# Performance work log

Hardware: AMD Instinct MI355X
Metric: run time of the kernel (lower is better)

## Reference

```python
import jax, jax.numpy as jnp
import numpy as np

B, S, D, H = 2, 2048, 1024, 16
HD = D // H

def setup_inputs() -> dict:
    key = jax.random.key(0)
    k1, k2, k3, k4, k5 = jax.random.split(key, 5)
    X = jax.random.normal(k1, (B, S, D), dtype=jnp.float32)
    # nn.Linear(D, 3D): weight [3D, D], bias [3D]
    W_qkv = jax.random.normal(k2, (3 * D, D), dtype=jnp.float32) * (1.0 / np.sqrt(D))
    b_qkv = jax.random.normal(k3, (3 * D,), dtype=jnp.float32) * 0.02
    W_out = jax.random.normal(k4, (D, D), dtype=jnp.float32) * (1.0 / np.sqrt(D))
    b_out = jax.random.normal(k5, (D,), dtype=jnp.float32) * 0.02
    return {"X": X, "W_qkv": W_qkv, "b_qkv": b_qkv, "W_out": W_out, "b_out": b_out}

def reference(X, W_qkv, b_qkv, W_out, b_out):
    b, s, d = X.shape
    qkv = jnp.einsum('bsd,ed->bse', X, W_qkv) + b_qkv  # [B,S,3D]
    q, k, v = jnp.split(qkv, 3, axis=2)
    def heads(t):
        return t.reshape(b, s, H, HD).transpose(0, 2, 1, 3)  # [B,H,S,HD]
    q, k, v = heads(q), heads(k), heads(v)
    scores = jnp.einsum('bhqd,bhkd->bhqk', q, k) * (1.0 / np.sqrt(HD))
    causal = jnp.tril(jnp.ones((s, s), dtype=bool))
    scores = jnp.where(causal[None, None], scores, jnp.float32(-jnp.inf))
    probs = jax.nn.softmax(scores, axis=-1)
    attn = jnp.einsum('bhqk,bhkd->bhqd', probs, v)  # [B,H,S,HD]
    attn = attn.transpose(0, 2, 1, 3).reshape(b, s, d)
    out = jnp.einsum('bsd,ed->bse', attn, W_out) + b_out
    return out
```

## Files before the change

kernel.cpp:

```cpp
#include <hip/hip_runtime.h>


typedef _Float16 f16x8 __attribute__((ext_vector_type(8)));
typedef _Float16 f16x4 __attribute__((ext_vector_type(4)));
typedef float    f32x4 __attribute__((ext_vector_type(4)));
typedef unsigned short u16x8 __attribute__((ext_vector_type(8)));

__device__ __forceinline__ float bf16_bits_to_f32(unsigned short u) {
    union { unsigned int i; float f; } v; v.i = ((unsigned int)u) << 16; return v.f;
}
__device__ __forceinline__ unsigned short f32_to_bf16_bits(float f) {
    union { float f; unsigned int i; } v; v.f = f;
    unsigned int x = v.i;
    return (unsigned short)((x + 0x7fffu + ((x >> 16) & 1u)) >> 16);
}
__device__ __forceinline__ float fexp2(float x) {
#if __has_builtin(__builtin_amdgcn_exp2f)
    return __builtin_amdgcn_exp2f(x);
#else
    return exp2f(x);
#endif
}
__device__ __forceinline__ void gll16(const void* g, void* l) {
    __builtin_amdgcn_global_load_lds(
        (const __attribute__((address_space(1))) unsigned int*)g,
        (__attribute__((address_space(3))) unsigned int*)l, 16, 0, 0);
}

__device__ __forceinline__ bool wave_isf32(const void* in, size_t off, int wave, int lane) {
    const unsigned short* probe = (const unsigned short*)in + off + (size_t)wave * 128 + lane * 2;
    unsigned short u0 = probe[0], u1 = probe[1];
    bool hit = (((u0 >> 7) & 0xFFu) >= 0x90u) || (((u1 >> 7) & 0xFFu) >= 0x90u);
    return __any(hit);
}

__device__ __forceinline__ f16x8 cvt8(const void* in, size_t i, bool isf32) {
    f16x8 c;
    if (isf32) {
        const float4* p4 = (const float4*)((const float*)in + i);
        float4 a0 = p4[0], a1 = p4[1];
        c[0] = (_Float16)a0.x; c[1] = (_Float16)a0.y; c[2] = (_Float16)a0.z; c[3] = (_Float16)a0.w;
        c[4] = (_Float16)a1.x; c[5] = (_Float16)a1.y; c[6] = (_Float16)a1.z; c[7] = (_Float16)a1.w;
    } else {
        u16x8 r = *(const u16x8*)((const unsigned short*)in + i);
        #pragma unroll
        for (int j = 0; j < 8; j++) c[j] = (_Float16)bf16_bits_to_f32(r[j]);
    }
    return c;
}

__global__ void __launch_bounds__(256) cvt2s_kernel(const void* __restrict__ Wqkv, _Float16* __restrict__ wout,
                                                    const void* __restrict__ X, _Float16* __restrict__ xout,
                                                    unsigned int* __restrict__ flag) {
    int b = blockIdx.x;
    const void* in; _Float16* out; size_t off;
    if (b < 1536) { in = Wqkv; out = wout; off = (size_t)b * 2048; }
    else          { in = X;    out = xout; off = (size_t)(b - 1536) * 2048; }
    const int wave = threadIdx.x >> 6, lane = threadIdx.x & 63;
    const bool isf32 = wave_isf32(in, off, wave, lane);
    if (b == 0 && threadIdx.x == 0) flag[0] = isf32 ? 1u : 0u;
    size_t i = off + (size_t)threadIdx.x * 8;
    *(f16x8*)(out + i) = cvt8(in, i, isf32);
}

__global__ void __launch_bounds__(256) cvtws_kernel(const void* __restrict__ in,
                                                    _Float16* __restrict__ out,
                                                    unsigned int* __restrict__ flag, int wf) {
    size_t off = (size_t)blockIdx.x * 2048;
    const int wave = threadIdx.x >> 6, lane = threadIdx.x & 63;
    const bool isf32 = wave_isf32(in, off, wave, lane);
    if (wf && blockIdx.x == 0 && threadIdx.x == 0) flag[0] = isf32 ? 1u : 0u;
    size_t i = off + (size_t)threadIdx.x * 8;
    *(f16x8*)(out + i) = cvt8(in, i, isf32);
}

template<int AF16>
__global__ void __launch_bounds__(256) qkv_gemm(
    const void* __restrict__ A, const _Float16* __restrict__ Wf,
    const void* __restrict__ bias, const unsigned int* __restrict__ flag,
    _Float16* __restrict__ qws, _Float16* __restrict__ kws, _Float16* __restrict__ vtws)
{
    constexpr int AST = AF16 ? 32 : 56;
    __shared__ _Float16 As[128 * AST];
    __shared__ _Float16 Bs[128 * 32];
    const bool isf32 = (flag[0] != 0u);
    const int tid  = threadIdx.x;
    const int lane = tid & 63, wave = tid >> 6;
    const int l15  = lane & 15, quad = lane >> 4;
    const int wm   = (wave >> 1) * 64, wn = (wave & 1) * 64;
    const int m0   = blockIdx.y * 128, n0 = blockIdx.x * 128;
    const int srow = tid >> 1, scol = (tid & 1) * 16;

    f32x4 acc[4][4] = {};

    for (int k0 = 0; k0 < 1024; k0 += 32) {
        if (AF16) {
            #pragma unroll
            for (int i = 0; i < 2; i++) {
                int seg = (wave * 2 + i) * 64 + lane;
                int row = seg >> 2, qtr = seg & 3;
                gll16((const _Float16*)A + (size_t)(m0 + row) * 1024 + k0 + qtr * 8,
                      &As[(wave * 2 + i) * 512]);
            }
        } else {
            f16x8 c0, c1;
            if (isf32) {
                const float4* ga = (const float4*)((const float*)A + (size_t)(m0 + srow) * 1024 + k0 + scol);
                float4 a0 = ga[0], a1 = ga[1], a2 = ga[2], a3 = ga[3];
                c0[0]=(_Float16)a0.x; c0[1]=(_Float16)a0.y; c0[2]=(_Float16)a0.z; c0[3]=(_Float16)a0.w;
                c0[4]=(_Float16)a1.x; c0[5]=(_Float16)a1.y; c0[6]=(_Float16)a1.z; c0[7]=(_Float16)a1.w;
                c1[0]=(_Float16)a2.x; c1[1]=(_Float16)a2.y; c1[2]=(_Float16)a2.z; c1[3]=(_Float16)a2.w;
                c1[4]=(_Float16)a3.x; c1[5]=(_Float16)a3.y; c1[6]=(_Float16)a3.z; c1[7]=(_Float16)a3.w;
            } else {
                const unsigned short* ga = (const unsigned short*)A + (size_t)(m0 + srow) * 1024 + k0 + scol;
                u16x8 r0 = *(const u16x8*)ga, r1 = *(const u16x8*)(ga + 8);
                #pragma unroll
                for (int i = 0; i < 8; i++) {
                    c0[i] = (_Float16)bf16_bits_to_f32(r0[i]);
                    c1[i] = (_Float16)bf16_bits_to_f32(r1[i]);
                }
            }
            *(f16x8*)&As[srow * AST + scol]     = c0;
            *(f16x8*)&As[srow * AST + scol + 8] = c1;
        }
        #pragma unroll
        for (int i = 0; i < 2; i++) {
            int seg = (wave * 2 + i) * 64 + lane;
            int row = seg >> 2, qtr = seg & 3;
            gll16(Wf + (size_t)(n0 + row) * 1024 + k0 + qtr * 8, &Bs[(wave * 2 + i) * 512]);
        }
        __syncthreads();
        f16x8 af[4], bfg[4];
        #pragma unroll
        for (int mt = 0; mt < 4; mt++)
            af[mt] = *(const f16x8*)&As[(wm + mt * 16 + l15) * AST + quad * 8];
        #pragma unroll
        for (int nt = 0; nt < 4; nt++)
            bfg[nt] = *(const f16x8*)&Bs[(wn + nt * 16 + l15) * 32 + quad * 8];
        #pragma unroll
        for (int mt = 0; mt < 4; mt++)
            #pragma unroll
            for (int nt = 0; nt < 4; nt++)
                acc[mt][nt] = __builtin_amdgcn_mfma_f32_16x16x32_f16(af[mt], bfg[nt], acc[mt][nt], 0, 0, 0);
        __syncthreads();
    }

    const float qsc = 0.18033688011112042591f;
    #pragma unroll
    for (int mt = 0; mt < 4; mt++) {
        #pragma unroll
        for (int nt = 0; nt < 4; nt++) {
            #pragma unroll
            for (int r = 0; r < 4; r++) {
                int m = m0 + wm + mt * 16 + quad * 4 + r;
                int n = n0 + wn + nt * 16 + l15;
                float bval = isf32 ? ((const float*)bias)[n] : bf16_bits_to_f32(((const unsigned short*)bias)[n]);
                float val = acc[mt][nt][r] + bval;
                int b = m >> 11, s = m & 2047;
                int t = n >> 10, e = n & 1023;
                int h = e >> 6, hd = e & 63;
                int bh = b * 16 + h;
                if (t == 0)      qws[((size_t)bh * 2048 + s) * 64 + hd]  = (_Float16)(val * qsc);
                else if (t == 1) kws[((size_t)bh * 2048 + s) * 64 + hd]  = (_Float16)val;
                else             vtws[((size_t)bh * 64 + hd) * 2048 + s] = (_Float16)val;
            }
        }
    }
}

__global__ void __launch_bounds__(256) out_gemm(
    const _Float16* __restrict__ Alo, const _Float16* __restrict__ Ahi,
    const _Float16* __restrict__ Wf, const void* __restrict__ bias,
    const unsigned int* __restrict__ flag, void* __restrict__ outp, int m_base)
{
    __shared__ _Float16 As[64 * 32];
    __shared__ _Float16 Bs[64 * 32];
    const bool isf32 = (flag[0] != 0u);
    const int tid  = threadIdx.x;
    const int lane = tid & 63, wave = tid >> 6;
    const int l15  = lane & 15, quad = lane >> 4;
    const int wm   = (wave >> 1) * 32, wn = (wave & 1) * 32;
    const int m0g  = m_base + blockIdx.y * 64, n0 = blockIdx.x * 64;
    const _Float16* A = (m0g < 2048) ? (Alo + (size_t)m0g * 1024)
                                     : (Ahi + (size_t)(m0g - 2048) * 1024);
    f32x4 acc[2][2] = {};

    for (int k0 = 0; k0 < 1024; k0 += 32) {
        {
            int row = tid >> 2, qtr = tid & 3;
            gll16(A + (size_t)row * 1024 + k0 + qtr * 8, &As[tid * 8]);
            gll16(Wf + (size_t)(n0 + row) * 1024 + k0 + qtr * 8, &Bs[tid * 8]);
        }
        __syncthreads();
        f16x8 af[2], bfg[2];
        #pragma unroll
        for (int mt = 0; mt < 2; mt++)
            af[mt] = *(const f16x8*)&As[(wm + mt * 16 + l15) * 32 + quad * 8];
        #pragma unroll
        for (int nt = 0; nt < 2; nt++)
            bfg[nt] = *(const f16x8*)&Bs[(wn + nt * 16 + l15) * 32 + quad * 8];
        #pragma unroll
        for (int mt = 0; mt < 2; mt++)
            #pragma unroll
            for (int nt = 0; nt < 2; nt++)
                acc[mt][nt] = __builtin_amdgcn_mfma_f32_16x16x32_f16(af[mt], bfg[nt], acc[mt][nt], 0, 0, 0);
        __syncthreads();
    }

    #pragma unroll
    for (int mt = 0; mt < 2; mt++) {
        #pragma unroll
        for (int nt = 0; nt < 2; nt++) {
            #pragma unroll
            for (int r = 0; r < 4; r++) {
                int m = m0g + wm + mt * 16 + quad * 4 + r;
                int n = n0 + wn + nt * 16 + l15;
                float bval = isf32 ? ((const float*)bias)[n] : bf16_bits_to_f32(((const unsigned short*)bias)[n]);
                float val = acc[mt][nt][r] + bval;
                size_t idx = (size_t)m * 1024 + n;
                if (isf32) ((float*)outp)[idx] = val;
                else       ((unsigned short*)outp)[idx] = f32_to_bf16_bits(val);
            }
        }
    }
}

__global__ void __launch_bounds__(256) flash_kernel(
    const _Float16* __restrict__ qws,
    const _Float16* __restrict__ kws,
    const _Float16* __restrict__ vtws,
    _Float16* __restrict__ attn_lo,
    _Float16* __restrict__ attn_hi)
{
    __shared__ _Float16 Ks[2][64 * 64];
    __shared__ _Float16 Vs[2][64 * 72];

    const int bh   = blockIdx.x;
    const int qb   = 31 - blockIdx.y;
    const int tid  = threadIdx.x;
    const int wave = tid >> 6;
    const int lane = tid & 63;
    const int l15  = lane & 15, quad = lane >> 4;

    const _Float16* Q  = qws  + (size_t)bh * 2048 * 64;
    const _Float16* Kp = kws  + (size_t)bh * 2048 * 64;
    const _Float16* Vt = vtws + (size_t)bh * 64 * 2048;

    const int q0w = qb * 64 + wave * 16;
    f16x8 qf0 = *(const f16x8*)(Q + (size_t)(q0w + l15) * 64 + quad * 8);
    f16x8 qf1 = *(const f16x8*)(Q + (size_t)(q0w + l15) * 64 + 32 + quad * 8);

    f32x4 o[4] = {};
    float lp = 0.f;
    const int nch = qb + 1;

    {
        #pragma unroll
        for (int i = 0; i < 2; i++) {
            int s = (wave * 2 + i) * 64 + lane;
            int row = s >> 3, cs = ((s & 7) - row) & 7;
            gll16(Kp + (size_t)row * 64 + cs * 8, &Ks[0][s * 8]);
        }
        int hd = tid >> 3, ko = (tid & 7) * 8;
        f16x8 v0 = *(const f16x8*)(Vt + (size_t)hd * 2048 + ko);
        f16x8 v1 = *(const f16x8*)(Vt + (size_t)(hd + 32) * 2048 + ko);
        *(f16x8*)&Vs[0][hd * 72 + ko]        = v0;
        *(f16x8*)&Vs[0][(hd + 32) * 72 + ko] = v1;
    }

    for (int c = 0; c < nch; c++) {
        __syncthreads();
        const int cb = c & 1;
        const bool more = (c + 1 < nch);
        f16x8 vr0, vr1;
        int hd = tid >> 3, ko = (tid & 7) * 8;
        if (more) {
            int jn = (c + 1) * 64;
            vr0 = *(const f16x8*)(Vt + (size_t)hd * 2048 + jn + ko);
            vr1 = *(const f16x8*)(Vt + (size_t)(hd + 32) * 2048 + jn + ko);
            #pragma unroll
            for (int i = 0; i < 2; i++) {
                int s = (wave * 2 + i) * 64 + lane;
                int row = s >> 3, cs = ((s & 7) - row) & 7;
                gll16(Kp + (size_t)(jn + row) * 64 + cs * 8, &Ks[cb ^ 1][s * 8]);
            }
        }

        const bool diag = (c == qb);
        f32x4 t[4];
        #pragma unroll
        for (int kt = 0; kt < 4; kt++) {
            int row = kt * 16 + l15;
            f16x8 k0 = *(const f16x8*)&Ks[cb][row * 64 + ((quad + l15) & 7) * 8];
            f16x8 k1 = *(const f16x8*)&Ks[cb][row * 64 + ((4 + quad + l15) & 7) * 8];
            f32x4 z = {};
            z = __builtin_amdgcn_mfma_f32_16x16x32_f16(k0, qf0, z, 0, 0, 0);
            t[kt] = __builtin_amdgcn_mfma_f32_16x16x32_f16(k1, qf1, z, 0, 0, 0);
        }
        float p[16];
        #pragma unroll
        for (int kt = 0; kt < 4; kt++)
            #pragma unroll
            for (int r = 0; r < 4; r++) {
                float v = t[kt][r];
                if (diag)
                    v = ((kt * 16 + quad * 4 + r) <= (wave * 16 + l15)) ? v : -INFINITY;
                p[kt * 4 + r] = fminf(fexp2(v), 60000.0f);
            }
        float rs = 0.f;
        #pragma unroll
        for (int i = 0; i < 16; i++) rs += p[i];
        lp += rs;
        f16x4 pf[4];
        #pragma unroll
        for (int kt = 0; kt < 4; kt++)
            #pragma unroll
            for (int r = 0; r < 4; r++) pf[kt][r] = (_Float16)p[kt * 4 + r];
        #pragma unroll
        for (int kt = 0; kt < 4; kt++) {
            #pragma unroll
            for (int mt = 0; mt < 4; mt++) {
                f16x4 cv = *(const f16x4*)&Vs[cb][(mt * 16 + l15) * 72 + kt * 16 + quad * 4];
                o[mt] = __builtin_amdgcn_mfma_f32_16x16x16f16(cv, pf[kt], o[mt], 0, 0, 0);
            }
        }

        if (more) {
            *(f16x8*)&Vs[cb ^ 1][hd * 72 + ko]        = vr0;
            *(f16x8*)&Vs[cb ^ 1][(hd + 32) * 72 + ko] = vr1;
        }
    }

    const int b = bh >> 4, h = bh & 15;
    _Float16* attn = (b == 0) ? attn_lo : attn_hi;
    {
        float rs = lp;
        rs += __shfl_xor(rs, 16);
        rs += __shfl_xor(rs, 32);
        const float inv = 1.0f / rs;
        const int s = q0w + l15;
        #pragma unroll
        for (int mt = 0; mt < 4; mt++) {
            #pragma unroll
            for (int r = 0; r < 4; r++) {
                int hdd = mt * 16 + quad * 4 + r;
                attn[(size_t)s * 1024 + h * 64 + hdd] = (_Float16)(o[mt][r] * inv);
            }
        }
    }
}

extern "C" void kernel_launch(void* const* d_in, const int* in_sizes, int n_in,
                              void* d_out, int out_size, void* d_ws, size_t ws_size,
                              hipStream_t stream) {
    (void)out_size;
    const void *X = nullptr, *Wqkv = nullptr, *bqkv = nullptr, *Wout = nullptr, *bout = nullptr;
    for (int i = 0; i < n_in; i++) {
        switch (in_sizes[i]) {
            case 4194304: X    = d_in[i]; break;
            case 3145728: Wqkv = d_in[i]; break;
            case 3072:    bqkv = d_in[i]; break;
            case 1048576: Wout = d_in[i]; break;
            case 1024:    bout = d_in[i]; break;
        }
    }
    char* ws = (char*)d_ws;
    const size_t MB = 1u << 20;
    unsigned int* flag = (unsigned int*)ws;
    char* base = ws + 256;

    if (ws_size >= (size_t)(385 * MB / 10)) {
        _Float16* wf16 = (_Float16*)(base);
        _Float16* xf16 = (_Float16*)(base + 6 * MB);
        _Float16* q    = (_Float16*)(base + 14 * MB);
        _Float16* k    = (_Float16*)(base + 22 * MB);
        _Float16* vt   = (_Float16*)(base + 30 * MB);
        cvt2s_kernel<<<dim3(3584), 256, 0, stream>>>(Wqkv, wf16, X, xf16, flag);
        qkv_gemm<1><<<dim3(24, 32), 256, 0, stream>>>(xf16, wf16, bqkv, flag, q, k, vt);
        cvtws_kernel<<<dim3(512), 256, 0, stream>>>(Wout, wf16, flag, 0);
        _Float16* attn = xf16;
        flash_kernel<<<dim3(32, 32), 256, 0, stream>>>(q, k, vt, attn, attn + (size_t)2048 * 1024);
        out_gemm<<<dim3(16, 64), 256, 0, stream>>>(attn, attn + (size_t)2048 * 1024,
                                                   wf16, bout, flag, d_out, 0);
    } else {
        _Float16* wf16    = (_Float16*)(base);
        _Float16* attn_hi = (_Float16*)(base + 6 * MB);
        _Float16* q       = (_Float16*)(base + 10 * MB);
        _Float16* k       = (_Float16*)(base + 18 * MB);
        _Float16* vt      = (_Float16*)(base + 26 * MB);
        _Float16* attn_lo = (_Float16*)((char*)d_out + 8 * MB);
        cvtws_kernel<<<dim3(1536), 256, 0, stream>>>(Wqkv, wf16, flag, 1);
        qkv_gemm<0><<<dim3(24, 32), 256, 0, stream>>>(X, wf16, bqkv, flag, q, k, vt);
        cvtws_kernel<<<dim3(512), 256, 0, stream>>>(Wout, wf16, flag, 0);
        flash_kernel<<<dim3(32, 32), 256, 0, stream>>>(q, k, vt, attn_lo, attn_hi);
        out_gemm<<<dim3(16, 32), 256, 0, stream>>>(attn_lo, attn_hi, wf16, bout, flag, d_out, 0);
        out_gemm<<<dim3(16, 32), 256, 0, stream>>>(attn_lo, attn_hi, wf16, bout, flag, d_out, 2048);
    }
}
```

Measured before the change: 190.9 us.

## Halve flash query tile and fuse W_out conversion into out_gemm loads

```diff
diff --git a/kernel.cpp b/kernel.cpp
--- a/kernel.cpp
+++ b/kernel.cpp
@@ -170,7 +170,7 @@
 
 __global__ void __launch_bounds__(256) out_gemm(
     const _Float16* __restrict__ Alo, const _Float16* __restrict__ Ahi,
-    const _Float16* __restrict__ Wf, const void* __restrict__ bias,
+    const void* __restrict__ W, const void* __restrict__ bias,
     const unsigned int* __restrict__ flag, void* __restrict__ outp, int m_base)
 {
     __shared__ _Float16 As[64 * 32];
@@ -185,12 +185,12 @@
                                      : (Ahi + (size_t)(m0g - 2048) * 1024);
     f32x4 acc[2][2] = {};
 
+    const int srow = tid >> 2, sqtr = tid & 3;
+
     for (int k0 = 0; k0 < 1024; k0 += 32) {
-        {
-            int row = tid >> 2, qtr = tid & 3;
-            gll16(A + (size_t)row * 1024 + k0 + qtr * 8, &As[tid * 8]);
-            gll16(Wf + (size_t)(n0 + row) * 1024 + k0 + qtr * 8, &Bs[tid * 8]);
-        }
+        gll16(A + (size_t)srow * 1024 + k0 + sqtr * 8, &As[tid * 8]);
+        f16x8 bw = cvt8(W, (size_t)(n0 + srow) * 1024 + k0 + sqtr * 8, isf32);
+        *(f16x8*)&Bs[tid * 8] = bw;
         __syncthreads();
         f16x8 af[2], bfg[2];
         #pragma unroll
@@ -225,18 +225,18 @@
     }
 }
 
-__global__ void __launch_bounds__(256) flash_kernel(
+__global__ void __launch_bounds__(128) flash_kernel(
     const _Float16* __restrict__ qws,
     const _Float16* __restrict__ kws,
     const _Float16* __restrict__ vtws,
     _Float16* __restrict__ attn_lo,
     _Float16* __restrict__ attn_hi)
 {
-    __shared__ _Float16 Ks[2][64 * 64];
-    __shared__ _Float16 Vs[2][64 * 72];
+    __shared__ _Float16 Ks[64 * 64];
+    __shared__ _Float16 Vs[64 * 72];
 
     const int bh   = blockIdx.x;
-    const int qb   = 31 - blockIdx.y;
+    const int qb   = 63 - blockIdx.y;
     const int tid  = threadIdx.x;
     const int wave = tid >> 6;
     const int lane = tid & 63;
@@ -246,53 +246,54 @@
     const _Float16* Kp = kws  + (size_t)bh * 2048 * 64;
     const _Float16* Vt = vtws + (size_t)bh * 64 * 2048;
 
-    const int q0w = qb * 64 + wave * 16;
+    const int q0w = qb * 32 + wave * 16;
     f16x8 qf0 = *(const f16x8*)(Q + (size_t)(q0w + l15) * 64 + quad * 8);
     f16x8 qf1 = *(const f16x8*)(Q + (size_t)(q0w + l15) * 64 + 32 + quad * 8);
 
     f32x4 o[4] = {};
     float lp = 0.f;
-    const int nch = qb + 1;
-
-    {
-        #pragma unroll
-        for (int i = 0; i < 2; i++) {
-            int s = (wave * 2 + i) * 64 + lane;
+    const int nch = qb / 2 + 1;
+
+    f16x8 vr[4];
+    #pragma unroll
+    for (int i = 0; i < 4; i++) {
+        int idx = i * 128 + tid, hd = idx >> 3, ks = idx & 7;
+        vr[i] = *(const f16x8*)(Vt + (size_t)hd * 2048 + ks * 8);
+    }
+
+    for (int c = 0; c < nch; c++) {
+        if (c) __syncthreads();
+        #pragma unroll
+        for (int i = 0; i < 4; i++) {
+            int idx = i * 128 + tid, hd = idx >> 3, ks = idx & 7;
+            *(f16x8*)&Vs[hd * 72 + ks * 8] = vr[i];
+        }
+        #pragma unroll
+        for (int i = 0; i < 4; i++) {
+            int s = i * 128 + tid;
             int row = s >> 3, cs = ((s & 7) - row) & 7;
-            gll16(Kp + (size_t)row * 64 + cs * 8, &Ks[0][s * 8]);
-        }
-        int hd = tid >> 3, ko = (tid & 7) * 8;
-        f16x8 v0 = *(const f16x8*)(Vt + (size_t)hd * 2048 + ko);
-        f16x8 v1 = *(const f16x8*)(Vt + (size_t)(hd + 32) * 2048 + ko);
-        *(f16x8*)&Vs[0][hd * 72 + ko]        = v0;
-        *(f16x8*)&Vs[0][(hd + 32) * 72 + ko] = v1;
-    }
-
-    for (int c = 0; c < nch; c++) {
-        __syncthreads();
-        const int cb = c & 1;
+            gll16(Kp + (size_t)(c * 64 + row) * 64 + cs * 8, &Ks[s * 8]);
+        }
+        __syncthreads();
+
         const bool more = (c + 1 < nch);
-        f16x8 vr0, vr1;
-        int hd = tid >> 3, ko = (tid & 7) * 8;
         if (more) {
             int jn = (c + 1) * 64;
-            vr0 = *(const f16x8*)(Vt + (size_t)hd * 2048 + jn + ko);
-            vr1 = *(const f16x8*)(Vt + (size_t)(hd + 32) * 2048 + jn + ko);
-            #pragma unroll
-            for (int i = 0; i < 2; i++) {
-                int s = (wave * 2 + i) * 64 + lane;
-                int row = s >> 3, cs = ((s & 7) - row) & 7;
-                gll16(Kp + (size_t)(jn + row) * 64 + cs * 8, &Ks[cb ^ 1][s * 8]);
-            }
-        }
-
-        const bool diag = (c == qb);
+            #pragma unroll
+            for (int i = 0; i < 4; i++) {
+                int idx = i * 128 + tid, hd = idx >> 3, ks = idx & 7;
+                vr[i] = *(const f16x8*)(Vt + (size_t)hd * 2048 + jn + ks * 8);
+            }
+        }
+
+        const int tb = q0w - c * 64;
+        const bool full = (tb >= 63);
         f32x4 t[4];
         #pragma unroll
         for (int kt = 0; kt < 4; kt++) {
             int row = kt * 16 + l15;
-            f16x8 k0 = *(const f16x8*)&Ks[cb][row * 64 + ((quad + l15) & 7) * 8];
-            f16x8 k1 = *(const f16x8*)&Ks[cb][row * 64 + ((4 + quad + l15) & 7) * 8];
+            f16x8 k0 = *(const f16x8*)&Ks[row * 64 + ((quad + l15) & 7) * 8];
+            f16x8 k1 = *(const f16x8*)&Ks[row * 64 + ((4 + quad + l15) & 7) * 8];
             f32x4 z = {};
             z = __builtin_amdgcn_mfma_f32_16x16x32_f16(k0, qf0, z, 0, 0, 0);
             t[kt] = __builtin_amdgcn_mfma_f32_16x16x32_f16(k1, qf1, z, 0, 0, 0);
@@ -303,8 +304,8 @@
             #pragma unroll
             for (int r = 0; r < 4; r++) {
                 float v = t[kt][r];
-                if (diag)
-                    v = ((kt * 16 + quad * 4 + r) <= (wave * 16 + l15)) ? v : -INFINITY;
+                if (!full)
+                    v = ((kt * 16 + quad * 4 + r) <= (tb + l15)) ? v : -INFINITY;
                 p[kt * 4 + r] = fminf(fexp2(v), 60000.0f);
             }
         float rs = 0.f;
@@ -320,14 +321,9 @@
         for (int kt = 0; kt < 4; kt++) {
             #pragma unroll
             for (int mt = 0; mt < 4; mt++) {
-                f16x4 cv = *(const f16x4*)&Vs[cb][(mt * 16 + l15) * 72 + kt * 16 + quad * 4];
+                f16x4 cv = *(const f16x4*)&Vs[(mt * 16 + l15) * 72 + kt * 16 + quad * 4];
                 o[mt] = __builtin_amdgcn_mfma_f32_16x16x16f16(cv, pf[kt], o[mt], 0, 0, 0);
             }
-        }
-
-        if (more) {
-            *(f16x8*)&Vs[cb ^ 1][hd * 72 + ko]        = vr0;
-            *(f16x8*)&Vs[cb ^ 1][(hd + 32) * 72 + ko] = vr1;
         }
     }
 
@@ -377,11 +373,10 @@
         _Float16* vt   = (_Float16*)(base + 30 * MB);
         cvt2s_kernel<<<dim3(3584), 256, 0, stream>>>(Wqkv, wf16, X, xf16, flag);
         qkv_gemm<1><<<dim3(24, 32), 256, 0, stream>>>(xf16, wf16, bqkv, flag, q, k, vt);
-        cvtws_kernel<<<dim3(512), 256, 0, stream>>>(Wout, wf16, flag, 0);
         _Float16* attn = xf16;
-        flash_kernel<<<dim3(32, 32), 256, 0, stream>>>(q, k, vt, attn, attn + (size_t)2048 * 1024);
+        flash_kernel<<<dim3(32, 64), 128, 0, stream>>>(q, k, vt, attn, attn + (size_t)2048 * 1024);
         out_gemm<<<dim3(16, 64), 256, 0, stream>>>(attn, attn + (size_t)2048 * 1024,
-                                                   wf16, bout, flag, d_out, 0);
+                                                   Wout, bout, flag, d_out, 0);
     } else {
         _Float16* wf16    = (_Float16*)(base);
         _Float16* attn_hi = (_Float16*)(base + 6 * MB);
@@ -391,9 +386,8 @@
         _Float16* attn_lo = (_Float16*)((char*)d_out + 8 * MB);
         cvtws_kernel<<<dim3(1536), 256, 0, stream>>>(Wqkv, wf16, flag, 1);
         qkv_gemm<0><<<dim3(24, 32), 256, 0, stream>>>(X, wf16, bqkv, flag, q, k, vt);
-        cvtws_kernel<<<dim3(512), 256, 0, stream>>>(Wout, wf16, flag, 0);
-        flash_kernel<<<dim3(32, 32), 256, 0, stream>>>(q, k, vt, attn_lo, attn_hi);
-        out_gemm<<<dim3(16, 32), 256, 0, stream>>>(attn_lo, attn_hi, wf16, bout, flag, d_out, 0);
-        out_gemm<<<dim3(16, 32), 256, 0, stream>>>(attn_lo, attn_hi, wf16, bout, flag, d_out, 2048);
-    }
-}
+        flash_kernel<<<dim3(32, 64), 128, 0, stream>>>(q, k, vt, attn_lo, attn_hi);
+        out_gemm<<<dim3(16, 32), 256, 0, stream>>>(attn_lo, attn_hi, Wout, bout, flag, d_out, 0);
+        out_gemm<<<dim3(16, 32), 256, 0, stream>>>(attn_lo, attn_hi, Wout, bout, flag, d_out, 2048);
+    }
+}
```

Measured after the change: 195.0 us. 2.1% more time.
